# Optimization experiments

Hardware: AMD Instinct MI355X
Metric: run time of the kernel (lower is better)

The kernel has to match this reference:

```python
import jax, jax.numpy as jnp
import numpy as np

N, E, IN_CH, HID, HEADS, OUT = 50000, 400000, 256, 128, 4, 2
EPS = 1e-5

def _bn(x, g, b):
    # training-mode BatchNorm1d (biased variance), dropout treated as eval (off)
    m = jnp.mean(x, axis=0)
    v = jnp.mean((x - m) ** 2, axis=0)
    return (x - m) * jax.lax.rsqrt(v + EPS) * g + b

def _sage(x, src, dst, Wl, bl, Wr):
    # PyG SAGEConv: lin_l(mean_{j->i} x_j) + lin_r(x_i)
    msg = jax.ops.segment_sum(x[src], dst, num_segments=N)
    deg = jax.ops.segment_sum(jnp.ones((src.shape[0],), x.dtype), dst, num_segments=N)
    agg = msg / jnp.maximum(deg, 1.0)[:, None]
    return agg @ Wl.T + bl + x @ Wr.T

def _gat(x, src, dst, W, a_s, a_d, bias):
    # PyG GATConv with self-loops already appended to (src, dst); concat heads
    d = W.shape[0] // HEADS
    xh = (x @ W.T).reshape(N, HEADS, d)
    asrc = jnp.einsum('nhd,hd->nh', xh, a_s)
    adst = jnp.einsum('nhd,hd->nh', xh, a_d)
    e = jax.nn.leaky_relu(asrc[src] + adst[dst], 0.2)          # [E+N, H]
    m = jax.ops.segment_max(e, dst, num_segments=N)            # segment softmax
    ex = jnp.exp(e - m[dst])
    den = jax.ops.segment_sum(ex, dst, num_segments=N)
    alpha = ex / den[dst]
    out = jax.ops.segment_sum(alpha[:, :, None] * xh[src], dst, num_segments=N)
    return out.reshape(N, HEADS * d) + bias

def setup_inputs():
    key = jax.random.key(0)
    ks = jax.random.split(key, 12)
    rnd = lambda k, s: jax.random.normal(k, s, dtype=jnp.float32) * 0.05
    H4 = HID * HEADS
    return {
        'x': jax.random.normal(ks[0], (N, IN_CH), dtype=jnp.float32),
        'edge_index': jax.random.randint(ks[1], (2, E), 0, N, dtype=jnp.int32),
        'W1l': rnd(ks[2], (HID, IN_CH)), 'b1': jnp.zeros((HID,), jnp.float32),
        'W1r': rnd(ks[3], (HID, IN_CH)),
        'g1': jnp.ones((HID,), jnp.float32), 'be1': jnp.zeros((HID,), jnp.float32),
        'Wg': rnd(ks[4], (H4, HID)),
        'a_src': rnd(ks[5], (HEADS, HID)), 'a_dst': rnd(ks[6], (HEADS, HID)),
        'gbias': jnp.zeros((H4,), jnp.float32),
        'g2': jnp.ones((H4,), jnp.float32), 'be2': jnp.zeros((H4,), jnp.float32),
        'W2l': rnd(ks[7], (HID, H4)), 'b2': jnp.zeros((HID,), jnp.float32),
        'W2r': rnd(ks[8], (HID, H4)),
        'g3': jnp.ones((HID,), jnp.float32), 'be3': jnp.zeros((HID,), jnp.float32),
        'Wf1': rnd(ks[9], (HID // 2, HID)), 'bf1': jnp.zeros((HID // 2,), jnp.float32),
        'g4': jnp.ones((HID // 2,), jnp.float32), 'be4': jnp.zeros((HID // 2,), jnp.float32),
        'Wf2': rnd(ks[10], (OUT, HID // 2)), 'bf2': jnp.zeros((OUT,), jnp.float32),
    }

def reference(x, edge_index, W1l, b1, W1r, g1, be1, Wg, a_src, a_dst, gbias,
              g2, be2, W2l, b2, W2r, g3, be3, Wf1, bf1, g4, be4, Wf2, bf2):
    src, dst = edge_index[0], edge_index[1]
    h = jax.nn.elu(_bn(_sage(x, src, dst, W1l, b1, W1r), g1, be1))
    loop = jnp.arange(N, dtype=src.dtype)                      # GAT adds self-loops
    src_sl = jnp.concatenate([src, loop])
    dst_sl = jnp.concatenate([dst, loop])
    h = jax.nn.elu(_bn(_gat(h, src_sl, dst_sl, Wg, a_src, a_dst, gbias), g2, be2))
    h = jax.nn.elu(_bn(_sage(h, src, dst, W2l, b2, W2r), g3, be3))
    h = jax.nn.elu(_bn(h @ Wf1.T + bf1, g4, be4))
    return h @ Wf2.T + bf2
```

## Files before the change

### kernel.cpp

```cpp
#include <hip/hip_runtime.h>
#include <cstdint>
#include <cstddef>

#define NN 50000
#define EE 400000
#define BN_EPS 1e-5f
#define NB_SCAN 196
#define NWAVE 8192
#define GB 784

typedef __attribute__((ext_vector_type(8))) short s16x8;
typedef __attribute__((ext_vector_type(4))) float floatx4;

__device__ __forceinline__ unsigned short f2b(float f) {
    uint32_t u = __float_as_uint(f);
    uint32_t r = (u + 0x7fffu + ((u >> 16) & 1u)) >> 16;
    return (unsigned short)r;
}
__device__ __forceinline__ uint32_t pack2(float a, float b) {
    return (uint32_t)f2b(a) | ((uint32_t)f2b(b) << 16);
}
__device__ __forceinline__ float b2f_lo(uint32_t u) { return __uint_as_float(u << 16); }
__device__ __forceinline__ float b2f_hi(uint32_t u) { return __uint_as_float(u & 0xffff0000u); }

#define GLD16(g, l) __builtin_amdgcn_global_load_lds(                          \
    (const __attribute__((address_space(1))) uint32_t*)(g),                    \
    (__attribute__((address_space(3))) uint32_t*)(l), 16, 0, 0)

__global__ __launch_bounds__(256)
void gemm_bf16mm(const unsigned short* __restrict__ A,
                 const unsigned short* __restrict__ W,
                 const float* __restrict__ bias,
                 unsigned short* __restrict__ Cb, float* __restrict__ Cf,
                 int split, int M, int K, int Ncol, int ldb, int ldf)
{
    __shared__ __align__(16) unsigned short As[128 * 32];
    __shared__ __align__(16) unsigned short Bs[128 * 32];
    const int t  = threadIdx.x;
    const int m0 = blockIdx.y * 128;
    const int n0 = blockIdx.x * 128;
    const int lane = t & 63;
    const int lr = lane & 15;
    const int lq = lane >> 4;
    const int wr = (t >> 7) * 64;
    const int wc = ((t >> 6) & 1) * 64;

    floatx4 acc[4][4];
    const floatx4 zero = {0.f, 0.f, 0.f, 0.f};
    #pragma unroll
    for (int i = 0; i < 4; ++i)
        #pragma unroll
        for (int j = 0; j < 4; ++j) acc[i][j] = zero;

    for (int k0 = 0; k0 < K; k0 += 32) {
        #pragma unroll
        for (int it = 0; it < 2; ++it) {
            const int seg  = t + it * 256;
            const int row  = seg >> 2;
            const int klog = (seg & 3) ^ ((row >> 1) & 3);
            const unsigned short* ga = A + (size_t)min(m0 + row, M - 1) * K + k0 + klog * 8;
            GLD16(ga, As + seg * 8);
            const unsigned short* gb = W + (size_t)min(n0 + row, Ncol - 1) * K + k0 + klog * 8;
            GLD16(gb, Bs + seg * 8);
        }
        __syncthreads();

        s16x8 af[4], bf[4];
        #pragma unroll
        for (int i = 0; i < 4; ++i) {
            const int ra = wr + i * 16 + lr;
            const int pa = lq ^ ((ra >> 1) & 3);
            af[i] = *(const s16x8*)(As + (ra * 4 + pa) * 8);
            const int rb = wc + i * 16 + lr;
            const int pb = lq ^ ((rb >> 1) & 3);
            bf[i] = *(const s16x8*)(Bs + (rb * 4 + pb) * 8);
        }
        #pragma unroll
        for (int i = 0; i < 4; ++i)
            #pragma unroll
            for (int j = 0; j < 4; ++j)
                acc[i][j] = __builtin_amdgcn_mfma_f32_16x16x32_bf16(
                    bf[j], af[i], acc[i][j], 0, 0, 0);
        __syncthreads();
    }

    const int orow = lane & 15;
    const int oc4  = (lane >> 4) * 4;
    #pragma unroll
    for (int i = 0; i < 4; ++i) {
        const int r = m0 + wr + i * 16 + orow;
        if (r >= M) continue;
        #pragma unroll
        for (int j = 0; j < 4; ++j) {
            const int cb = n0 + wc + j * 16 + oc4;
            if (cb >= Ncol) continue;
            const floatx4 a = acc[i][j];
            if (cb < split) {
                uint2 ov;
                ov.x = pack2(a[0], a[1]);
                ov.y = pack2(a[2], a[3]);
                *(uint2*)(Cb + (size_t)r * ldb + cb) = ov;
            } else {
                const int cc = cb - split;
                float4 o = make_float4(a[0], a[1], a[2], a[3]);
                if (bias) {
                    o.x += bias[cc]; o.y += bias[cc + 1];
                    o.z += bias[cc + 2]; o.w += bias[cc + 3];
                }
                *(float4*)(Cf + (size_t)r * ldf + cc) = o;
            }
        }
    }
}

__global__ __launch_bounds__(256)
void gemm_heads(const unsigned short* __restrict__ agg,
                const unsigned short* __restrict__ Wg,
                const float* __restrict__ gbias,
                unsigned short* __restrict__ out)
{
    __shared__ __align__(16) unsigned short As[128 * 32];
    __shared__ __align__(16) unsigned short Bs[128 * 32];
    const int t  = threadIdx.x;
    const int m0 = blockIdx.x * 128;
    const int h  = blockIdx.y;
    const int lane = t & 63;
    const int lr = lane & 15;
    const int lq = lane >> 4;
    const int wr = (t >> 7) * 64;
    const int wc = ((t >> 6) & 1) * 64;

    floatx4 acc[4][4];
    const floatx4 zero = {0.f, 0.f, 0.f, 0.f};
    #pragma unroll
    for (int i = 0; i < 4; ++i)
        #pragma unroll
        for (int j = 0; j < 4; ++j) acc[i][j] = zero;

    for (int k0 = 0; k0 < 128; k0 += 32) {
        #pragma unroll
        for (int it = 0; it < 2; ++it) {
            const int seg  = t + it * 256;
            const int row  = seg >> 2;
            const int klog = (seg & 3) ^ ((row >> 1) & 3);
            const unsigned short* ga = agg + (size_t)min(m0 + row, NN - 1) * 512 + h * 128 + k0 + klog * 8;
            GLD16(ga, As + seg * 8);
            const unsigned short* gb = Wg + (size_t)(h * 128 + row) * 128 + k0 + klog * 8;
            GLD16(gb, Bs + seg * 8);
        }
        __syncthreads();

        s16x8 af[4], bf[4];
        #pragma unroll
        for (int i = 0; i < 4; ++i) {
            const int ra = wr + i * 16 + lr;
            const int pa = lq ^ ((ra >> 1) & 3);
            af[i] = *(const s16x8*)(As + (ra * 4 + pa) * 8);
            const int rb = wc + i * 16 + lr;
            const int pb = lq ^ ((rb >> 1) & 3);
            bf[i] = *(const s16x8*)(Bs + (rb * 4 + pb) * 8);
        }
        #pragma unroll
        for (int i = 0; i < 4; ++i)
            #pragma unroll
            for (int j = 0; j < 4; ++j)
                acc[i][j] = __builtin_amdgcn_mfma_f32_16x16x32_bf16(
                    bf[j], af[i], acc[i][j], 0, 0, 0);
        __syncthreads();
    }

    const int orow = lane & 15;
    const int oc4  = (lane >> 4) * 4;
    #pragma unroll
    for (int i = 0; i < 4; ++i) {
        const int r = m0 + wr + i * 16 + orow;
        if (r >= NN) continue;
        #pragma unroll
        for (int j = 0; j < 4; ++j) {
            const int c = wc + j * 16 + oc4;
            const floatx4 a = acc[i][j];
            const float* gb = gbias + h * 128 + c;
            uint2 ov;
            ov.x = pack2(a[0] + gb[0], a[1] + gb[1]);
            ov.y = pack2(a[2] + gb[2], a[3] + gb[3]);
            *(uint2*)(out + (size_t)r * 512 + h * 128 + c) = ov;
        }
    }
}

__global__ void k_conv_x(const float* __restrict__ x, unsigned short* __restrict__ xb)
{
    const int i8 = (blockIdx.x * 256 + threadIdx.x) * 8;
    const float4 f0 = *(const float4*)(x + i8);
    const float4 f1 = *(const float4*)(x + i8 + 4);
    uint4 o;
    o.x = pack2(f0.x, f0.y); o.y = pack2(f0.z, f0.w);
    o.z = pack2(f1.x, f1.y); o.w = pack2(f1.z, f1.w);
    *(uint4*)(xb + i8) = o;
}

__global__ void k_conv_w(const float* __restrict__ s0, const float* __restrict__ s1,
                         const float* __restrict__ s2, const float* __restrict__ s3,
                         const float* __restrict__ s4, const float* __restrict__ s5,
                         unsigned short* __restrict__ dst)
{
    const int i = blockIdx.x * 256 + threadIdx.x;
    if (i >= 270336) return;
    float v;
    if      (i < 32768)  v = s0[i];
    else if (i < 65536)  v = s1[i - 32768];
    else if (i < 131072) v = s2[i - 65536];
    else if (i < 196608) v = s3[i - 131072];
    else if (i < 262144) v = s4[i - 196608];
    else                 v = s5[i - 262144];
    dst[i] = f2b(v);
}

__global__ void k_atilde(const float* __restrict__ a_s, const float* __restrict__ a_d,
                         const float* __restrict__ Wg, float* __restrict__ ats,
                         float* __restrict__ atd)
{
    const int k = threadIdx.x;
    const int h = blockIdx.x;
    float s = 0.f, d = 0.f;
    for (int j = 0; j < 128; ++j) {
        const float w = Wg[(size_t)(h * 128 + j) * 128 + k];
        s += a_s[h * 128 + j] * w;
        d += a_d[h * 128 + j] * w;
    }
    ats[h * 128 + k] = s;
    atd[h * 128 + k] = d;
}

__global__ void k_count(const int* __restrict__ dst, int* __restrict__ cnt)
{
    int i = blockIdx.x * blockDim.x + threadIdx.x;
    if (i < EE) atomicAdd(&cnt[dst[i]], 1);
}

__global__ __launch_bounds__(256)
void k_scan_blk(const int* __restrict__ cnt, int* __restrict__ offs,
                int* __restrict__ bsum, int N)
{
    __shared__ int wsum[4];
    const int t = threadIdx.x;
    const int i = blockIdx.x * 256 + t;
    const int v = (i < N) ? cnt[i] : 0;
    int s = v;
    #pragma unroll
    for (int o = 1; o < 64; o <<= 1) {
        const int u = __shfl_up(s, o);
        if ((t & 63) >= o) s += u;
    }
    const int wid = t >> 6;
    if ((t & 63) == 63) wsum[wid] = s;
    __syncthreads();
    int base = 0;
    #pragma unroll
    for (int w = 0; w < 3; ++w) if (w < wid) base += wsum[w];
    if (i < N) offs[i] = base + s - v;
    if (t == 255) bsum[blockIdx.x] = base + s;
}

__global__ __launch_bounds__(256)
void k_scan_top(int* __restrict__ bsum, int* __restrict__ offs, int N)
{
    __shared__ int wsum[4];
    const int t = threadIdx.x;
    const int v = (t < NB_SCAN) ? bsum[t] : 0;
    int s = v;
    #pragma unroll
    for (int o = 1; o < 64; o <<= 1) {
        const int u = __shfl_up(s, o);
        if ((t & 63) >= o) s += u;
    }
    const int wid = t >> 6;
    if ((t & 63) == 63) wsum[wid] = s;
    __syncthreads();
    int base = 0;
    #pragma unroll
    for (int w = 0; w < 3; ++w) if (w < wid) base += wsum[w];
    if (t < NB_SCAN) bsum[t] = base + s - v;
    if (t == 255) offs[N] = base + s;
}

__global__ __launch_bounds__(256)
void k_scan_add(int* __restrict__ offs, const int* __restrict__ bsum, int N)
{
    const int i = blockIdx.x * 256 + threadIdx.x;
    if (i < N) offs[i] += bsum[blockIdx.x];
}

__global__ void k_fill(const int* __restrict__ src, const int* __restrict__ dst,
                       const int* __restrict__ offs, int* __restrict__ fill,
                       int* __restrict__ csr)
{
    int i = blockIdx.x * blockDim.x + threadIdx.x;
    if (i < EE) {
        int d = dst[i];
        int p = offs[d] + atomicAdd(&fill[d], 1);
        csr[p] = src[i];
    }
}

__global__ __launch_bounds__(256)
void k_sage_agg(const unsigned short* __restrict__ tl, float* __restrict__ tr,
                const float* __restrict__ bias, const int* __restrict__ offs,
                const int* __restrict__ csr)
{
    const int l  = threadIdx.x & 63;
    const int g  = l >> 4;
    const int c0 = (l & 15) * 8;
    const int wv = blockIdx.x * 4 + (threadIdx.x >> 6);
    const float4 bv0 = *(const float4*)(bias + c0);
    const float4 bv1 = *(const float4*)(bias + c0 + 4);
    for (int nb = wv * 4; nb < NN; nb += NWAVE * 4) {
        const int n = nb + g;
        if (n < NN) {
            const int o0 = offs[n];
            const int deg = offs[n + 1] - o0;
            float a[8] = {0.f,0.f,0.f,0.f,0.f,0.f,0.f,0.f};
            for (int j = 0; j < deg; ++j) {
                const int sid = csr[o0 + j];
                const uint4 q = *(const uint4*)(tl + (size_t)sid * 128 + c0);
                a[0] += b2f_lo(q.x); a[1] += b2f_hi(q.x);
                a[2] += b2f_lo(q.y); a[3] += b2f_hi(q.y);
                a[4] += b2f_lo(q.z); a[5] += b2f_hi(q.z);
                a[6] += b2f_lo(q.w); a[7] += b2f_hi(q.w);
            }
            const float inv = 1.f / fmaxf((float)deg, 1.f);
            float* tp = tr + (size_t)n * 128 + c0;
            float4 t0 = *(float4*)tp;
            float4 t1 = *(float4*)(tp + 4);
            t0.x += a[0] * inv + bv0.x; t0.y += a[1] * inv + bv0.y;
            t0.z += a[2] * inv + bv0.z; t0.w += a[3] * inv + bv0.w;
            t1.x += a[4] * inv + bv1.x; t1.y += a[5] * inv + bv1.y;
            t1.z += a[6] * inv + bv1.z; t1.w += a[7] * inv + bv1.w;
            *(float4*)tp = t0;
            *(float4*)(tp + 4) = t1;
        }
    }
}

__global__ __launch_bounds__(256)
void k_attn_agg(const unsigned short* __restrict__ h1, const float* __restrict__ asrc,
                const float* __restrict__ adst, const int* __restrict__ offs,
                const int* __restrict__ csr, unsigned short* __restrict__ agg)
{
    const int l  = threadIdx.x & 63;
    const int g  = l >> 4;
    const int c0 = (l & 15) * 8;
    const int wv = blockIdx.x * 4 + (threadIdx.x >> 6);
    for (int nb = wv * 4; nb < NN; nb += NWAVE * 4) {
        const int n = nb + g;
        if (n >= NN) continue;
        const int o0 = offs[n];
        const int deg = offs[n + 1] - o0;
        const int total = deg + 1;
        const float4 adv = *(const float4*)(adst + n * 4);
        float den0 = 0.f, den1 = 0.f, den2 = 0.f, den3 = 0.f;
        float acc[4][8];
        #pragma unroll
        for (int h = 0; h < 4; ++h)
            #pragma unroll
            for (int i = 0; i < 8; ++i) acc[h][i] = 0.f;
        for (int j = 0; j < total; ++j) {
            const int sid = (j < deg) ? csr[o0 + j] : n;
            const float4 av = *(const float4*)(asrc + sid * 4);
            float e0 = av.x + adv.x, e1 = av.y + adv.y;
            float e2 = av.z + adv.z, e3 = av.w + adv.w;
            e0 = fmaxf(e0, 0.2f * e0); e1 = fmaxf(e1, 0.2f * e1);
            e2 = fmaxf(e2, 0.2f * e2); e3 = fmaxf(e3, 0.2f * e3);
            const float w0 = __expf(e0), w1 = __expf(e1);
            const float w2 = __expf(e2), w3 = __expf(e3);
            den0 += w0; den1 += w1; den2 += w2; den3 += w3;
            const uint4 q = *(const uint4*)(h1 + (size_t)sid * 128 + c0);
            float v[8];
            v[0] = b2f_lo(q.x); v[1] = b2f_hi(q.x);
            v[2] = b2f_lo(q.y); v[3] = b2f_hi(q.y);
            v[4] = b2f_lo(q.z); v[5] = b2f_hi(q.z);
            v[6] = b2f_lo(q.w); v[7] = b2f_hi(q.w);
            #pragma unroll
            for (int i = 0; i < 8; ++i) {
                acc[0][i] += w0 * v[i];
                acc[1][i] += w1 * v[i];
                acc[2][i] += w2 * v[i];
                acc[3][i] += w3 * v[i];
            }
        }
        const float r[4] = {1.f / den0, 1.f / den1, 1.f / den2, 1.f / den3};
        #pragma unroll
        for (int h = 0; h < 4; ++h) {
            uint4 ov;
            ov.x = pack2(acc[h][0] * r[h], acc[h][1] * r[h]);
            ov.y = pack2(acc[h][2] * r[h], acc[h][3] * r[h]);
            ov.z = pack2(acc[h][4] * r[h], acc[h][5] * r[h]);
            ov.w = pack2(acc[h][6] * r[h], acc[h][7] * r[h]);
            *(uint4*)(agg + (size_t)n * 512 + h * 128 + c0) = ov;
        }
    }
}

__global__ __launch_bounds__(64)
void k_statsA_f2(const float* __restrict__ X, float* __restrict__ P)
{
    const int c = threadIdx.x * 2;
    const int b = blockIdx.x;
    const int r0 = b * 64;
    const int r1 = min(r0 + 64, NN);
    float s0 = 0.f, s1 = 0.f, q0 = 0.f, q1 = 0.f;
    for (int r = r0; r < r1; ++r) {
        const float2 v = *(const float2*)(X + (size_t)r * 128 + c);
        s0 += v.x; q0 += v.x * v.x;
        s1 += v.y; q1 += v.y * v.y;
    }
    *(float2*)(P + (size_t)b * 256 + c) = make_float2(s0, s1);
    *(float2*)(P + (size_t)b * 256 + 128 + c) = make_float2(q0, q1);
}

__global__ __launch_bounds__(256)
void k_statsA_b2(const unsigned short* __restrict__ X, float* __restrict__ P)
{
    const int c = threadIdx.x * 2;
    const int b = blockIdx.x;
    const int r0 = b * 64;
    const int r1 = min(r0 + 64, NN);
    float s0 = 0.f, s1 = 0.f, q0 = 0.f, q1 = 0.f;
    for (int r = r0; r < r1; ++r) {
        const uint32_t u = *(const uint32_t*)(X + (size_t)r * 512 + c);
        const float v0 = b2f_lo(u), v1 = b2f_hi(u);
        s0 += v0; q0 += v0 * v0;
        s1 += v1; q1 += v1 * v1;
    }
    *(float2*)(P + (size_t)b * 1024 + c) = make_float2(s0, s1);
    *(float2*)(P + (size_t)b * 1024 + 512 + c) = make_float2(q0, q1);
}

__global__ __launch_bounds__(64)
void k_statsA_f(const float* __restrict__ X, float* __restrict__ P)
{
    const int c = threadIdx.x;
    const int b = blockIdx.x;
    const int r0 = b * 64;
    const int r1 = min(r0 + 64, NN);
    float s = 0.f, q = 0.f;
    for (int r = r0; r < r1; ++r) {
        const float v = X[(size_t)r * 64 + c];
        s += v; q += v * v;
    }
    P[(size_t)b * 128 + c] = s;
    P[(size_t)b * 128 + 64 + c] = q;
}

template<int CHUNK>
__global__ void k_bn_reduce(const float* __restrict__ P, int C,
                            const float* __restrict__ g, const float* __restrict__ be,
                            float* __restrict__ scale, float* __restrict__ shift)
{
    __shared__ float sb[8 * CHUNK];
    __shared__ float qb[8 * CHUNK];
    const int t = threadIdx.x;
    const int cl = t & (CHUNK - 1);
    const int grp = t / CHUNK;
    const int c = blockIdx.x * CHUNK + cl;
    float s = 0.f, q = 0.f;
    for (int b = grp; b < GB; b += 8) {
        s += P[(size_t)b * 2 * C + c];
        q += P[(size_t)b * 2 * C + C + c];
    }
    sb[grp * CHUNK + cl] = s;
    qb[grp * CHUNK + cl] = q;
    __syncthreads();
    if (t < CHUNK) {
        float S = 0.f, Q = 0.f;
        #pragma unroll
        for (int g2 = 0; g2 < 8; ++g2) { S += sb[g2 * CHUNK + t]; Q += qb[g2 * CHUNK + t]; }
        const int cc = blockIdx.x * CHUNK + t;
        const float mean = S / (float)NN;
        float var = Q / (float)NN - mean * mean;
        var = fmaxf(var, 0.f);
        const float sc = g[cc] * rsqrtf(var + BN_EPS);
        scale[cc] = sc;
        shift[cc] = be[cc] - mean * sc;
    }
}

__global__ void k_bn_elu_f2b(const float* __restrict__ X, unsigned short* __restrict__ D,
                             const float* __restrict__ scale, const float* __restrict__ shift,
                             int Cm1, int total)
{
    const int i = (blockIdx.x * 256 + threadIdx.x) * 4;
    if (i >= total) return;
    const int c = i & Cm1;
    const float4 x = *(const float4*)(X + i);
    float o[4] = {x.x, x.y, x.z, x.w};
    #pragma unroll
    for (int k = 0; k < 4; ++k) {
        const float v = o[k] * scale[c + k] + shift[c + k];
        o[k] = (v > 0.f) ? v : (__expf(v) - 1.f);
    }
    uint2 ov;
    ov.x = pack2(o[0], o[1]); ov.y = pack2(o[2], o[3]);
    *(uint2*)(D + i) = ov;
}

__global__ void k_bn_elu_b2b(unsigned short* __restrict__ X,
                             const float* __restrict__ scale, const float* __restrict__ shift,
                             int Cm1, int total)
{
    const int i = (blockIdx.x * 256 + threadIdx.x) * 4;
    if (i >= total) return;
    const int c = i & Cm1;
    const uint2 u = *(const uint2*)(X + i);
    float o[4] = {b2f_lo(u.x), b2f_hi(u.x), b2f_lo(u.y), b2f_hi(u.y)};
    #pragma unroll
    for (int k = 0; k < 4; ++k) {
        const float v = o[k] * scale[c + k] + shift[c + k];
        o[k] = (v > 0.f) ? v : (__expf(v) - 1.f);
    }
    uint2 ov;
    ov.x = pack2(o[0], o[1]); ov.y = pack2(o[2], o[3]);
    *(uint2*)(X + i) = ov;
}

__global__ __launch_bounds__(256)
void k_bn_elu_coef(const float* __restrict__ X, unsigned short* __restrict__ D,
                   const float* __restrict__ scale, const float* __restrict__ shift,
                   const float* __restrict__ ats, const float* __restrict__ atd,
                   float* __restrict__ asrc, float* __restrict__ adst)
{
    const int l = threadIdx.x & 63;
    const int wv = blockIdx.x * 4 + (threadIdx.x >> 6);
    const int c = l * 2;
    const float2 sc = *(const float2*)(scale + c);
    const float2 sh = *(const float2*)(shift + c);
    float2 sa[4], da[4];
    #pragma unroll
    for (int h = 0; h < 4; ++h) {
        sa[h] = *(const float2*)(ats + h * 128 + c);
        da[h] = *(const float2*)(atd + h * 128 + c);
    }
    for (int n = wv; n < NN; n += NWAVE) {
        const float2 xv = *(const float2*)(X + (size_t)n * 128 + c);
        float v0 = xv.x * sc.x + sh.x;
        float v1 = xv.y * sc.y + sh.y;
        v0 = (v0 > 0.f) ? v0 : (__expf(v0) - 1.f);
        v1 = (v1 > 0.f) ? v1 : (__expf(v1) - 1.f);
        const uint32_t p = pack2(v0, v1);
        *(uint32_t*)(D + (size_t)n * 128 + c) = p;
        const float r0 = b2f_lo(p), r1 = b2f_hi(p);
        float ps[4], pd[4];
        #pragma unroll
        for (int h = 0; h < 4; ++h) {
            ps[h] = r0 * sa[h].x + r1 * sa[h].y;
            pd[h] = r0 * da[h].x + r1 * da[h].y;
        }
        #pragma unroll
        for (int o = 1; o < 64; o <<= 1) {
            #pragma unroll
            for (int h = 0; h < 4; ++h) {
                ps[h] += __shfl_xor(ps[h], o);
                pd[h] += __shfl_xor(pd[h], o);
            }
        }
        if (l == 0) {
            *(float4*)(asrc + n * 4) = make_float4(ps[0], ps[1], ps[2], ps[3]);
            *(float4*)(adst + n * 4) = make_float4(pd[0], pd[1], pd[2], pd[3]);
        }
    }
}

__global__ __launch_bounds__(256)
void k_bn_elu_fc2(const float* __restrict__ X, const float* __restrict__ scale,
                  const float* __restrict__ shift, const float* __restrict__ W,
                  const float* __restrict__ bias, float* __restrict__ out)
{
    const int c = threadIdx.x & 63;
    const int gw = blockIdx.x * 4 + (threadIdx.x >> 6);
    const float sc = scale[c], sh = shift[c];
    const float w0 = W[c], w1 = W[64 + c];
    const float b0 = bias[0], b1 = bias[1];
    for (int n = gw; n < NN; n += NWAVE) {
        float v = X[(size_t)n * 64 + c] * sc + sh;
        v = (v > 0.f) ? v : (__expf(v) - 1.f);
        float p0 = v * w0;
        float p1 = v * w1;
        #pragma unroll
        for (int o = 1; o < 64; o <<= 1) {
            p0 += __shfl_xor(p0, o);
            p1 += __shfl_xor(p1, o);
        }
        if (c == 0) {
            out[n * 2 + 0] = p0 + b0;
            out[n * 2 + 1] = p1 + b1;
        }
    }
}

extern "C" void kernel_launch(void* const* d_in, const int* in_sizes, int n_in,
                              void* d_out, int out_size, void* d_ws, size_t ws_size,
                              hipStream_t stream)
{
    const float* x     = (const float*)d_in[0];
    const int*   ei    = (const int*)d_in[1];
    const float* W1l   = (const float*)d_in[2];
    const float* b1    = (const float*)d_in[3];
    const float* W1r   = (const float*)d_in[4];
    const float* g1    = (const float*)d_in[5];
    const float* be1   = (const float*)d_in[6];
    const float* Wg    = (const float*)d_in[7];
    const float* a_s   = (const float*)d_in[8];
    const float* a_d   = (const float*)d_in[9];
    const float* gbias = (const float*)d_in[10];
    const float* g2    = (const float*)d_in[11];
    const float* be2   = (const float*)d_in[12];
    const float* W2l   = (const float*)d_in[13];
    const float* b2    = (const float*)d_in[14];
    const float* W2r   = (const float*)d_in[15];
    const float* g3    = (const float*)d_in[16];
    const float* be3   = (const float*)d_in[17];
    const float* Wf1   = (const float*)d_in[18];
    const float* bf1   = (const float*)d_in[19];
    const float* g4    = (const float*)d_in[20];
    const float* be4   = (const float*)d_in[21];
    const float* Wf2   = (const float*)d_in[22];
    const float* bf2   = (const float*)d_in[23];
    const int* src = ei;
    const int* dst = ei + EE;

    char* ws = (char*)d_ws;
    size_t off = 0;
    auto alloc = [&](size_t bytes) -> char* {
        char* p = ws + off;
        off += (bytes + 255) & ~(size_t)255;
        return p;
    };
    unsigned short* xb   = (unsigned short*)alloc((size_t)NN * 256 * 2);
    unsigned short* waren= (unsigned short*)alloc(270336 * 2);
    unsigned short* tlb  = (unsigned short*)alloc((size_t)NN * 128 * 2);
    float*          trF  = (float*)alloc((size_t)NN * 128 * 4);
    unsigned short* h1b  = (unsigned short*)alloc((size_t)NN * 128 * 2);
    unsigned short* aggb = (unsigned short*)alloc((size_t)NN * 512 * 2);
    unsigned short* gatb = (unsigned short*)alloc((size_t)NN * 512 * 2);
    float* asrc  = (float*)alloc((size_t)NN * 4 * 4);
    float* adst  = (float*)alloc((size_t)NN * 4 * 4);
    float* ats   = (float*)alloc(512 * 4);
    float* atd   = (float*)alloc(512 * 4);
    float* pstat = (float*)alloc((size_t)GB * 1024 * 4);
    float* scsh  = (float*)alloc(1024 * 4);
    int*   cntfill = (int*)alloc((size_t)NN * 2 * 4);
    int*   offs  = (int*)alloc((size_t)(NN + 1) * 4);
    int*   csr   = (int*)alloc((size_t)EE * 4);
    int*   bsum  = (int*)alloc((size_t)NB_SCAN * 4);
    if (off > ws_size) return;
    (void)in_sizes; (void)n_in; (void)out_size;

    unsigned short* W1cat = waren;
    unsigned short* Wg_b  = waren + 65536;
    unsigned short* W2cat = waren + 131072;
    unsigned short* Wf1_b = waren + 262144;

    int* cnt  = cntfill;
    int* fill = cntfill + NN;
    float* scale = scsh;
    float* shift = scsh + 512;

    k_conv_x<<<6250, 256, 0, stream>>>(x, xb);
    k_conv_w<<<1056, 256, 0, stream>>>(W1l, W1r, Wg, W2l, W2r, Wf1, waren);
    k_atilde<<<4, 128, 0, stream>>>(a_s, a_d, Wg, ats, atd);
    hipMemsetAsync(cntfill, 0, (size_t)NN * 2 * 4, stream);
    k_count<<<(EE + 255) / 256, 256, 0, stream>>>(dst, cnt);
    k_scan_blk<<<NB_SCAN, 256, 0, stream>>>(cnt, offs, bsum, NN);
    k_scan_top<<<1, 256, 0, stream>>>(bsum, offs, NN);
    k_scan_add<<<NB_SCAN, 256, 0, stream>>>(offs, bsum, NN);
    k_fill<<<(EE + 255) / 256, 256, 0, stream>>>(src, dst, offs, fill, csr);

    const int gy = (NN + 127) / 128;

    gemm_bf16mm<<<dim3(2, gy), 256, 0, stream>>>(xb, W1cat, nullptr, tlb, trF,
                                                 128, NN, 256, 256, 128, 128);
    k_sage_agg<<<2048, 256, 0, stream>>>(tlb, trF, b1, offs, csr);
    k_statsA_f2<<<GB, 64, 0, stream>>>(trF, pstat);
    k_bn_reduce<128><<<1, 1024, 0, stream>>>(pstat, 128, g1, be1, scale, shift);
    k_bn_elu_coef<<<2048, 256, 0, stream>>>(trF, h1b, scale, shift, ats, atd, asrc, adst);

    k_attn_agg<<<2048, 256, 0, stream>>>(h1b, asrc, adst, offs, csr, aggb);
    gemm_heads<<<dim3(gy, 4), 256, 0, stream>>>(aggb, Wg_b, gbias, gatb);
    k_statsA_b2<<<GB, 256, 0, stream>>>(gatb, pstat);
    k_bn_reduce<128><<<4, 1024, 0, stream>>>(pstat, 512, g2, be2, scale, shift);
    k_bn_elu_b2b<<<(NN * 512 / 4 + 255) / 256, 256, 0, stream>>>(gatb, scale, shift, 511, NN * 512);

    gemm_bf16mm<<<dim3(2, gy), 256, 0, stream>>>(gatb, W2cat, nullptr, tlb, trF,
                                                 128, NN, 512, 256, 128, 128);
    k_sage_agg<<<2048, 256, 0, stream>>>(tlb, trF, b2, offs, csr);
    k_statsA_f2<<<GB, 64, 0, stream>>>(trF, pstat);
    k_bn_reduce<128><<<1, 1024, 0, stream>>>(pstat, 128, g3, be3, scale, shift);
    k_bn_elu_f2b<<<(NN * 128 / 4 + 255) / 256, 256, 0, stream>>>(trF, h1b, scale, shift, 127, NN * 128);

    gemm_bf16mm<<<dim3(1, gy), 256, 0, stream>>>(h1b, Wf1_b, bf1, nullptr, trF,
                                                 0, NN, 128, 64, 0, 64);
    k_statsA_f<<<GB, 64, 0, stream>>>(trF, pstat);
    k_bn_reduce<64><<<1, 512, 0, stream>>>(pstat, 64, g4, be4, scale, shift);

    k_bn_elu_fc2<<<2048, 256, 0, stream>>>(trF, scale, shift, Wf2, bf2, (float*)d_out);
}
```

Before: 645.0 us.

## Fuse BN statistics into SAGE aggregation and widen concat GEMM tile

The SAGE aggregation kernel now accumulates per-channel sum and sum-of-squares in registers and writes per-block partials, so the separate statistics pass that re-read the fp32 output is gone. The BN reduce kernel takes the partial-block count as a parameter to handle the new 2048-block partials. A new GEMM variant computes both the 128-wide lin_l and lin_r halves in one 128x256 block, so the A tile is loaded once instead of twice. This trades one kernel launch and one full read of trF for higher register pressure in the GEMM (32 accumulator vectors per thread) and some extra work in the aggregation kernel.

```diff
diff --git a/kernel.cpp b/kernel.cpp
--- a/kernel.cpp
+++ b/kernel.cpp
@@ -8,6 +8,7 @@
 #define NB_SCAN 196
 #define NWAVE 8192
 #define GB 784
+#define GAGG 2048
 
 typedef __attribute__((ext_vector_type(8))) short s16x8;
 typedef __attribute__((ext_vector_type(4))) float floatx4;
@@ -26,6 +27,98 @@
 #define GLD16(g, l) __builtin_amdgcn_global_load_lds(                          \
     (const __attribute__((address_space(1))) uint32_t*)(g),                    \
     (__attribute__((address_space(3))) uint32_t*)(l), 16, 0, 0)
+
+__global__ __launch_bounds__(256)
+void gemm_w256(const unsigned short* __restrict__ A,
+               const unsigned short* __restrict__ W,
+               unsigned short* __restrict__ Cb, float* __restrict__ Cf,
+               int M, int K)
+{
+    __shared__ __align__(16) unsigned short As[128 * 32];
+    __shared__ __align__(16) unsigned short Bs[256 * 32];
+    const int t  = threadIdx.x;
+    const int m0 = blockIdx.x * 128;
+    const int lane = t & 63;
+    const int lr = lane & 15;
+    const int lq = lane >> 4;
+    const int wid = t >> 6;
+    const int wr  = (wid >> 1) * 64;
+    const int wc2 = (wid & 1) * 128;
+
+    floatx4 acc[4][8];
+    const floatx4 zero = {0.f, 0.f, 0.f, 0.f};
+    #pragma unroll
+    for (int i = 0; i < 4; ++i)
+        #pragma unroll
+        for (int j = 0; j < 8; ++j) acc[i][j] = zero;
+
+    for (int k0 = 0; k0 < K; k0 += 32) {
+        #pragma unroll
+        for (int it = 0; it < 2; ++it) {
+            const int seg  = t + it * 256;
+            const int row  = seg >> 2;
+            const int klog = (seg & 3) ^ ((row >> 1) & 3);
+            const unsigned short* ga = A + (size_t)min(m0 + row, M - 1) * K + k0 + klog * 8;
+            GLD16(ga, As + seg * 8);
+        }
+        #pragma unroll
+        for (int it = 0; it < 4; ++it) {
+            const int seg  = t + it * 256;
+            const int row  = seg >> 2;
+            const int klog = (seg & 3) ^ ((row >> 1) & 3);
+            const unsigned short* gb = W + (size_t)row * K + k0 + klog * 8;
+            GLD16(gb, Bs + seg * 8);
+        }
+        __syncthreads();
+
+        s16x8 af[4], bf[8];
+        #pragma unroll
+        for (int i = 0; i < 4; ++i) {
+            const int ra = wr + i * 16 + lr;
+            const int pa = lq ^ ((ra >> 1) & 3);
+            af[i] = *(const s16x8*)(As + (ra * 4 + pa) * 8);
+        }
+        #pragma unroll
+        for (int j = 0; j < 8; ++j) {
+            const int rb = wc2 + j * 16 + lr;
+            const int pb = lq ^ ((rb >> 1) & 3);
+            bf[j] = *(const s16x8*)(Bs + (rb * 4 + pb) * 8);
+        }
+        #pragma unroll
+        for (int i = 0; i < 4; ++i)
+            #pragma unroll
+            for (int j = 0; j < 8; ++j)
+                acc[i][j] = __builtin_amdgcn_mfma_f32_16x16x32_bf16(
+                    bf[j], af[i], acc[i][j], 0, 0, 0);
+        __syncthreads();
+    }
+
+    const int orow = lane & 15;
+    const int oc4  = (lane >> 4) * 4;
+    #pragma unroll
+    for (int i = 0; i < 4; ++i) {
+        const int r = m0 + wr + i * 16 + orow;
+        if (r >= M) continue;
+        if (wc2 == 0) {
+            #pragma unroll
+            for (int j = 0; j < 8; ++j) {
+                const int c = j * 16 + oc4;
+                const floatx4 a = acc[i][j];
+                uint2 ov;
+                ov.x = pack2(a[0], a[1]);
+                ov.y = pack2(a[2], a[3]);
+                *(uint2*)(Cb + (size_t)r * 128 + c) = ov;
+            }
+        } else {
+            #pragma unroll
+            for (int j = 0; j < 8; ++j) {
+                const int c = j * 16 + oc4;
+                const floatx4 a = acc[i][j];
+                *(float4*)(Cf + (size_t)r * 128 + c) = make_float4(a[0], a[1], a[2], a[3]);
+            }
+        }
+    }
+}
 
 __global__ __launch_bounds__(256)
 void gemm_bf16mm(const unsigned short* __restrict__ A,
@@ -306,14 +399,18 @@
 __global__ __launch_bounds__(256)
 void k_sage_agg(const unsigned short* __restrict__ tl, float* __restrict__ tr,
                 const float* __restrict__ bias, const int* __restrict__ offs,
-                const int* __restrict__ csr)
-{
+                const int* __restrict__ csr, float* __restrict__ P)
+{
+    __shared__ float red[4][256];
     const int l  = threadIdx.x & 63;
     const int g  = l >> 4;
     const int c0 = (l & 15) * 8;
-    const int wv = blockIdx.x * 4 + (threadIdx.x >> 6);
+    const int wid = threadIdx.x >> 6;
+    const int wv = blockIdx.x * 4 + wid;
     const float4 bv0 = *(const float4*)(bias + c0);
     const float4 bv1 = *(const float4*)(bias + c0 + 4);
+    float ps[8] = {0.f,0.f,0.f,0.f,0.f,0.f,0.f,0.f};
+    float qs[8] = {0.f,0.f,0.f,0.f,0.f,0.f,0.f,0.f};
     for (int nb = wv * 4; nb < NN; nb += NWAVE * 4) {
         const int n = nb + g;
         if (n < NN) {
@@ -332,14 +429,33 @@
             float* tp = tr + (size_t)n * 128 + c0;
             float4 t0 = *(float4*)tp;
             float4 t1 = *(float4*)(tp + 4);
-            t0.x += a[0] * inv + bv0.x; t0.y += a[1] * inv + bv0.y;
-            t0.z += a[2] * inv + bv0.z; t0.w += a[3] * inv + bv0.w;
-            t1.x += a[4] * inv + bv1.x; t1.y += a[5] * inv + bv1.y;
-            t1.z += a[6] * inv + bv1.z; t1.w += a[7] * inv + bv1.w;
-            *(float4*)tp = t0;
-            *(float4*)(tp + 4) = t1;
-        }
-    }
+            float v[8];
+            v[0] = t0.x + a[0] * inv + bv0.x; v[1] = t0.y + a[1] * inv + bv0.y;
+            v[2] = t0.z + a[2] * inv + bv0.z; v[3] = t0.w + a[3] * inv + bv0.w;
+            v[4] = t1.x + a[4] * inv + bv1.x; v[5] = t1.y + a[5] * inv + bv1.y;
+            v[6] = t1.z + a[6] * inv + bv1.z; v[7] = t1.w + a[7] * inv + bv1.w;
+            *(float4*)tp       = make_float4(v[0], v[1], v[2], v[3]);
+            *(float4*)(tp + 4) = make_float4(v[4], v[5], v[6], v[7]);
+            #pragma unroll
+            for (int i = 0; i < 8; ++i) { ps[i] += v[i]; qs[i] += v[i] * v[i]; }
+        }
+    }
+    #pragma unroll
+    for (int i = 0; i < 8; ++i) {
+        ps[i] += __shfl_xor(ps[i], 16); ps[i] += __shfl_xor(ps[i], 32);
+        qs[i] += __shfl_xor(qs[i], 16); qs[i] += __shfl_xor(qs[i], 32);
+    }
+    if (l < 16) {
+        #pragma unroll
+        for (int i = 0; i < 8; ++i) {
+            red[wid][c0 + i]       = ps[i];
+            red[wid][128 + c0 + i] = qs[i];
+        }
+    }
+    __syncthreads();
+    const int tc = threadIdx.x;
+    const float s = red[0][tc] + red[1][tc] + red[2][tc] + red[3][tc];
+    P[(size_t)blockIdx.x * 256 + tc] = s;
 }
 
 __global__ __launch_bounds__(256)
@@ -401,23 +517,6 @@
     }
 }
 
-__global__ __launch_bounds__(64)
-void k_statsA_f2(const float* __restrict__ X, float* __restrict__ P)
-{
-    const int c = threadIdx.x * 2;
-    const int b = blockIdx.x;
-    const int r0 = b * 64;
-    const int r1 = min(r0 + 64, NN);
-    float s0 = 0.f, s1 = 0.f, q0 = 0.f, q1 = 0.f;
-    for (int r = r0; r < r1; ++r) {
-        const float2 v = *(const float2*)(X + (size_t)r * 128 + c);
-        s0 += v.x; q0 += v.x * v.x;
-        s1 += v.y; q1 += v.y * v.y;
-    }
-    *(float2*)(P + (size_t)b * 256 + c) = make_float2(s0, s1);
-    *(float2*)(P + (size_t)b * 256 + 128 + c) = make_float2(q0, q1);
-}
-
 __global__ __launch_bounds__(256)
 void k_statsA_b2(const unsigned short* __restrict__ X, float* __restrict__ P)
 {
@@ -453,7 +552,7 @@
 }
 
 template<int CHUNK>
-__global__ void k_bn_reduce(const float* __restrict__ P, int C,
+__global__ void k_bn_reduce(const float* __restrict__ P, int C, int nb,
                             const float* __restrict__ g, const float* __restrict__ be,
                             float* __restrict__ scale, float* __restrict__ shift)
 {
@@ -464,7 +563,7 @@
     const int grp = t / CHUNK;
     const int c = blockIdx.x * CHUNK + cl;
     float s = 0.f, q = 0.f;
-    for (int b = grp; b < GB; b += 8) {
+    for (int b = grp; b < nb; b += 8) {
         s += P[(size_t)b * 2 * C + c];
         q += P[(size_t)b * 2 * C + C + c];
     }
@@ -646,7 +745,8 @@
     float* adst  = (float*)alloc((size_t)NN * 4 * 4);
     float* ats   = (float*)alloc(512 * 4);
     float* atd   = (float*)alloc(512 * 4);
-    float* pstat = (float*)alloc((size_t)GB * 1024 * 4);
+    float* pstat = (float*)alloc((size_t)GAGG * 256 * 4 > (size_t)GB * 1024 * 4
+                                 ? (size_t)GAGG * 256 * 4 : (size_t)GB * 1024 * 4);
     float* scsh  = (float*)alloc(1024 * 4);
     int*   cntfill = (int*)alloc((size_t)NN * 2 * 4);
     int*   offs  = (int*)alloc((size_t)(NN + 1) * 4);
@@ -677,30 +777,26 @@
 
     const int gy = (NN + 127) / 128;
 
-    gemm_bf16mm<<<dim3(2, gy), 256, 0, stream>>>(xb, W1cat, nullptr, tlb, trF,
-                                                 128, NN, 256, 256, 128, 128);
-    k_sage_agg<<<2048, 256, 0, stream>>>(tlb, trF, b1, offs, csr);
-    k_statsA_f2<<<GB, 64, 0, stream>>>(trF, pstat);
-    k_bn_reduce<128><<<1, 1024, 0, stream>>>(pstat, 128, g1, be1, scale, shift);
+    gemm_w256<<<gy, 256, 0, stream>>>(xb, W1cat, tlb, trF, NN, 256);
+    k_sage_agg<<<GAGG, 256, 0, stream>>>(tlb, trF, b1, offs, csr, pstat);
+    k_bn_reduce<128><<<1, 1024, 0, stream>>>(pstat, 128, GAGG, g1, be1, scale, shift);
     k_bn_elu_coef<<<2048, 256, 0, stream>>>(trF, h1b, scale, shift, ats, atd, asrc, adst);
 
     k_attn_agg<<<2048, 256, 0, stream>>>(h1b, asrc, adst, offs, csr, aggb);
     gemm_heads<<<dim3(gy, 4), 256, 0, stream>>>(aggb, Wg_b, gbias, gatb);
     k_statsA_b2<<<GB, 256, 0, stream>>>(gatb, pstat);
-    k_bn_reduce<128><<<4, 1024, 0, stream>>>(pstat, 512, g2, be2, scale, shift);
+    k_bn_reduce<128><<<4, 1024, 0, stream>>>(pstat, 512, GB, g2, be2, scale, shift);
     k_bn_elu_b2b<<<(NN * 512 / 4 + 255) / 256, 256, 0, stream>>>(gatb, scale, shift, 511, NN * 512);
 
-    gemm_bf16mm<<<dim3(2, gy), 256, 0, stream>>>(gatb, W2cat, nullptr, tlb, trF,
-                                                 128, NN, 512, 256, 128, 128);
-    k_sage_agg<<<2048, 256, 0, stream>>>(tlb, trF, b2, offs, csr);
-    k_statsA_f2<<<GB, 64, 0, stream>>>(trF, pstat);
-    k_bn_reduce<128><<<1, 1024, 0, stream>>>(pstat, 128, g3, be3, scale, shift);
+    gemm_w256<<<gy, 256, 0, stream>>>(gatb, W2cat, tlb, trF, NN, 512);
+    k_sage_agg<<<GAGG, 256, 0, stream>>>(tlb, trF, b2, offs, csr, pstat);
+    k_bn_reduce<128><<<1, 1024, 0, stream>>>(pstat, 128, GAGG, g3, be3, scale, shift);
     k_bn_elu_f2b<<<(NN * 128 / 4 + 255) / 256, 256, 0, stream>>>(trF, h1b, scale, shift, 127, NN * 128);
 
     gemm_bf16mm<<<dim3(1, gy), 256, 0, stream>>>(h1b, Wf1_b, bf1, nullptr, trF,
                                                  0, NN, 128, 64, 0, 64);
     k_statsA_f<<<GB, 64, 0, stream>>>(trF, pstat);
-    k_bn_reduce<64><<<1, 512, 0, stream>>>(pstat, 64, g4, be4, scale, shift);
+    k_bn_reduce<64><<<1, 512, 0, stream>>>(pstat, 64, GB, g4, be4, scale, shift);
 
     k_bn_elu_fc2<<<2048, 256, 0, stream>>>(trF, scale, shift, Wf2, bf2, (float*)d_out);
 }
```

Result: slower. 696.2 us (+7.9%).
